# Optimization experiments

Hardware: AMD Instinct MI355X
Metric: run time of the kernel (lower is better)

Reference implementation:

```python
import jax, jax.numpy as jnp
import numpy as np

B, M, F_IN = 512, 256, 128
HID = 128          # g_feature_out_n entries
N_GL = 4           # number of GraphMatLayers
INT_D = 128
FINAL_D = 1024
OUT_DIM = 1
N_RB = 3           # ResNet block_sizes=[3]
SCALE = 0.02


def setup_inputs() -> dict:
    key = jax.random.key(0)
    ks = jax.random.split(key, 20)
    d = {}
    d['G'] = jax.random.normal(ks[0], (B, 1, M, M), dtype=jnp.float32)
    d['x_G'] = jax.random.normal(ks[1], (B, M, F_IN), dtype=jnp.float32)
    # GraphMatLayer linear weights (torch nn.Linear: [out, in]), all 128->128
    d['gml_W'] = jax.random.normal(ks[2], (N_GL, HID, F_IN), dtype=jnp.float32) * SCALE
    d['gml_b'] = jax.random.normal(ks[3], (N_GL, HID), dtype=jnp.float32) * SCALE
    d['lin0_W'] = jax.random.normal(ks[4], (INT_D, HID), dtype=jnp.float32) * SCALE
    d['lin0_b'] = jax.random.normal(ks[5], (INT_D,), dtype=jnp.float32) * SCALE
    d['rin_W'] = jax.random.normal(ks[6], (INT_D, INT_D), dtype=jnp.float32) * SCALE
    d['rin_b'] = jax.random.normal(ks[7], (INT_D,), dtype=jnp.float32) * SCALE
    d['rb1_W'] = jax.random.normal(ks[8], (N_RB, INT_D, INT_D), dtype=jnp.float32) * SCALE
    d['rb1_b'] = jax.random.normal(ks[9], (N_RB, INT_D), dtype=jnp.float32) * SCALE
    d['rb2_W'] = jax.random.normal(ks[10], (N_RB, INT_D, INT_D), dtype=jnp.float32) * SCALE
    d['rout_W'] = jax.random.normal(ks[11], (INT_D, INT_D), dtype=jnp.float32) * SCALE
    d['rout_b'] = jax.random.normal(ks[12], (INT_D,), dtype=jnp.float32) * SCALE
    d['f1_W'] = jax.random.normal(ks[13], (FINAL_D, INT_D), dtype=jnp.float32) * SCALE
    d['f1_b'] = jax.random.normal(ks[14], (FINAL_D,), dtype=jnp.float32) * SCALE
    d['f2_W'] = jax.random.normal(ks[15], (OUT_DIM, FINAL_D), dtype=jnp.float32) * SCALE
    d['f2_b'] = jax.random.normal(ks[16], (OUT_DIM,), dtype=jnp.float32) * SCALE
    return d


def reference(G, x_G, gml_W, gml_b, lin0_W, lin0_b, rin_W, rin_b,
              rb1_W, rb1_b, rb2_W, rout_W, rout_b, f1_W, f1_b, f2_W, f2_b):
    # GS=1: G[:, 0] is the per-graph adjacency [B, M, M].
    # Note: with GS=1 the torch code's resnet shape check never matches
    # (extra singleton dims accumulate), so there are NO residuals in gml.
    G0 = G[:, 0]
    x = x_G  # [B, M, C]
    for l in range(gml_W.shape[0]):  # static small loop over layers
        y = x @ gml_W[l].T + gml_b[l]             # linear projection [B,M,P]
        x = jax.nn.relu(jnp.einsum('bmn,bnp->bmp', G0, y))
    h = x.reshape(-1, x.shape[-1])                # [B*M, HID]
    h = h @ lin0_W.T + lin0_b                     # Linear(D, INT_D)
    h = h @ rin_W.T + rin_b                       # ResNet.linear_in
    for i in range(rb1_W.shape[0]):               # 3 residual blocks
        h = h + jax.nn.relu(h @ rb1_W[i].T + rb1_b[i]) @ rb2_W[i].T
    h = h @ rout_W.T + rout_b                     # ResNet.linear_out
    h = jax.nn.relu(h @ f1_W.T + f1_b)            # Linear(INT_D, FINAL_D) + ReLU
    out = h @ f2_W.T + f2_b                       # Linear(FINAL_D, OUT_DIM)
    return out.reshape(G.shape[0], G.shape[2], -1)  # [B, M, OUT_DIM]
```

## Files before the change

kernel.cpp:

```cpp
#include <hip/hip_runtime.h>


typedef __attribute__((ext_vector_type(8))) __bf16 bf16x8;
typedef __attribute__((ext_vector_type(4))) float f32x4;
typedef __attribute__((ext_vector_type(4))) unsigned short us4;
typedef __attribute__((ext_vector_type(8))) unsigned short us8;

#define MFMA16(a, b, c) __builtin_amdgcn_mfma_f32_16x16x32_bf16((a), (b), (c), 0, 0, 0)

__device__ __forceinline__ unsigned short f2bf(float f) {
  unsigned u = __float_as_uint(f);
  return (unsigned short)((u + 0x7fffu + ((u >> 16) & 1u)) >> 16);
}
__device__ __forceinline__ float bf2f(unsigned short s) {
  return __uint_as_float(((unsigned)s) << 16);
}
__device__ __forceinline__ bf16x8 asb(us8 u) { return __builtin_bit_cast(bf16x8, u); }

__device__ __forceinline__ us8 cvt8(f32x4 a, f32x4 c) {
  us8 r;
  r[0] = f2bf(a[0]); r[1] = f2bf(a[1]); r[2] = f2bf(a[2]); r[3] = f2bf(a[3]);
  r[4] = f2bf(c[0]); r[5] = f2bf(c[1]); r[6] = f2bf(c[2]); r[7] = f2bf(c[3]);
  return r;
}

__device__ __forceinline__ bf16x8 lds_frag(const unsigned short* p) {
  return asb(*reinterpret_cast<const us8*>(p));
}

struct WReg { f32x4 a[4]; f32x4 b[4]; };

__device__ __forceinline__ void stage_load(WReg& w, const float* __restrict__ src, int tid) {
#pragma unroll
  for (int it = 0; it < 4; ++it) {
    int o = tid + it * 512;
    int p = o >> 4;
    int f = (o & 15) << 3;
    const float* s = src + p * 128 + f;
    w.a[it] = *reinterpret_cast<const f32x4*>(s);
    w.b[it] = *reinterpret_cast<const f32x4*>(s + 4);
  }
}

__device__ __forceinline__ void stage_store(const WReg& w, unsigned short* dst, int tid) {
#pragma unroll
  for (int it = 0; it < 4; ++it) {
    int o = tid + it * 512;
    int p = o >> 4;
    int f = (o & 15) << 3;
    *reinterpret_cast<us8*>(&dst[p * 128 + (f ^ ((p & 7) << 3))]) = cvt8(w.a[it], w.b[it]);
  }
}

__global__ __launch_bounds__(512, 2)
void fused_model(const float* __restrict__ G, const float* __restrict__ xG,
                 const float* __restrict__ gmlW, const float* __restrict__ gmlb,
                 const float* __restrict__ lin0W, const float* __restrict__ lin0b,
                 const float* __restrict__ rinW, const float* __restrict__ rinb,
                 const float* __restrict__ rb1W, const float* __restrict__ rb1b,
                 const float* __restrict__ rb2W,
                 const float* __restrict__ routW, const float* __restrict__ routb,
                 const float* __restrict__ f1W, const float* __restrict__ f1b,
                 const float* __restrict__ f2W, const float* __restrict__ f2b,
                 float* __restrict__ out)
{
  __shared__ __align__(16) unsigned short bufA[256 * 128];
  __shared__ __align__(16) unsigned short bufB[256 * 128];
  __shared__ __align__(16) unsigned short wls[128 * 128];

  const int tid = (int)threadIdx.x;
  const int b = (int)blockIdx.x;
  const int wv = tid >> 6;
  const int lane = tid & 63;
  const int lr = lane & 15;
  const int lg = lane >> 4;

  const f32x4 zero4 = {0.f, 0.f, 0.f, 0.f};
  WReg wreg;

  {
    const float* xb = xG + (size_t)b * (256 * 128);
#pragma unroll
    for (int it = 0; it < 8; ++it) {
      int o = tid + it * 512;
      int n = o >> 4;
      int f = (o & 15) << 3;
      const float* s = xb + n * 128 + f;
      f32x4 x0 = *reinterpret_cast<const f32x4*>(s);
      f32x4 x1 = *reinterpret_cast<const f32x4*>(s + 4);
      *reinterpret_cast<us8*>(&bufA[n * 128 + (f ^ ((n & 7) << 3))]) = cvt8(x0, x1);
    }
  }
  stage_load(wreg, gmlW, tid);
  stage_store(wreg, wls, tid);

  const float* Gb = G + (size_t)b * (256 * 256);
  bf16x8 bg[2][8];
#pragma unroll
  for (int mt = 0; mt < 2; ++mt) {
    int m = wv * 32 + mt * 16 + lr;
    const float* grow = Gb + (size_t)m * 256;
#pragma unroll
    for (int ks = 0; ks < 8; ++ks) {
      const float* s = grow + ks * 32 + lg * 8;
      f32x4 x0 = *reinterpret_cast<const f32x4*>(s);
      f32x4 x1 = *reinterpret_cast<const f32x4*>(s + 4);
      bg[mt][ks] = asb(cvt8(x0, x1));
    }
  }
  __syncthreads();

#pragma unroll 1
  for (int l = 0; l < 4; ++l) {
    {
      bf16x8 a[2][4];
#pragma unroll
      for (int nt = 0; nt < 2; ++nt) {
        int n = wv * 32 + nt * 16 + lr;
#pragma unroll
        for (int k = 0; k < 4; ++k)
          a[nt][k] = lds_frag(&bufA[n * 128 + ((k * 32 + lg * 8) ^ ((n & 7) << 3))]);
      }
      const float* bias = gmlb + l * 128;
#pragma unroll
      for (int ptg = 0; ptg < 8; ptg += 4) {
        f32x4 acc[4][2];
#pragma unroll
        for (int j = 0; j < 4; ++j) { acc[j][0] = zero4; acc[j][1] = zero4; }
#pragma unroll
        for (int k = 0; k < 4; ++k) {
#pragma unroll
          for (int j = 0; j < 4; ++j) {
            int p = (ptg + j) * 16 + lr;
            bf16x8 bw = lds_frag(&wls[p * 128 + ((k * 32 + lg * 8) ^ ((p & 7) << 3))]);
            acc[j][0] = MFMA16(a[0][k], bw, acc[j][0]);
            acc[j][1] = MFMA16(a[1][k], bw, acc[j][1]);
          }
        }
#pragma unroll
        for (int j = 0; j < 4; ++j) {
          int p = (ptg + j) * 16 + lr;
          float bv = bias[p];
#pragma unroll
          for (int nt = 0; nt < 2; ++nt) {
            int nb = wv * 32 + nt * 16 + lg * 4;
            us4 pk;
#pragma unroll
            for (int r = 0; r < 4; ++r) pk[r] = f2bf(acc[j][nt][r] + bv);
            *reinterpret_cast<us4*>(&bufB[p * 256 + (nb ^ ((p & 7) << 3))]) = pk;
          }
        }
      }
    }
    __syncthreads();

    stage_load(wreg, (l < 3) ? (gmlW + (l + 1) * 16384) : lin0W, tid);

    {
#pragma unroll
      for (int ptg = 0; ptg < 8; ptg += 2) {
        bf16x8 ya[2][8];
#pragma unroll
        for (int j = 0; j < 2; ++j) {
          int p = (ptg + j) * 16 + lr;
#pragma unroll
          for (int ks = 0; ks < 8; ++ks)
            ya[j][ks] = lds_frag(&bufB[p * 256 + ((ks * 32 + lg * 8) ^ ((p & 7) << 3))]);
        }
        f32x4 acc[2][2];
        acc[0][0] = zero4; acc[0][1] = zero4; acc[1][0] = zero4; acc[1][1] = zero4;
#pragma unroll
        for (int ks = 0; ks < 8; ++ks) {
#pragma unroll
          for (int j = 0; j < 2; ++j) {
            acc[j][0] = MFMA16(ya[j][ks], bg[0][ks], acc[j][0]);
            acc[j][1] = MFMA16(ya[j][ks], bg[1][ks], acc[j][1]);
          }
        }
#pragma unroll
        for (int j = 0; j < 2; ++j) {
#pragma unroll
          for (int mt = 0; mt < 2; ++mt) {
            int m = wv * 32 + mt * 16 + lr;
            int pb = (ptg + j) * 16 + lg * 4;
            us4 pk;
#pragma unroll
            for (int r = 0; r < 4; ++r) {
              float v = acc[j][mt][r];
              v = v > 0.f ? v : 0.f;
              pk[r] = f2bf(v);
            }
            *reinterpret_cast<us4*>(&bufA[m * 128 + (pb ^ ((m & 7) << 3))]) = pk;
          }
        }
      }
    }
    stage_store(wreg, wls, tid);
    __syncthreads();
  }

  stage_load(wreg, rinW, tid);
#pragma unroll 1
  for (int op = 0; op < 9; ++op) {
    const float* bp;
    const float* wn;
    bool rl = false, rs = false;
    switch (op) {
      case 0: bp = lin0b;      wn = rb1W;          break;
      case 1: bp = rinb;       wn = rb2W;          break;
      case 2: bp = rb1b;       wn = rb1W + 16384;  rl = true; break;
      case 3: bp = nullptr;    wn = rb2W + 16384;  rs = true; break;
      case 4: bp = rb1b + 128; wn = rb1W + 32768;  rl = true; break;
      case 5: bp = nullptr;    wn = rb2W + 32768;  rs = true; break;
      case 6: bp = rb1b + 256; wn = routW;         rl = true; break;
      case 7: bp = nullptr;    wn = f1W;           rs = true; break;
      default: bp = routb;     wn = nullptr;       break;
    }
    const unsigned short* s = (op & 1) ? bufB : bufA;
    unsigned short* d = (op & 1) ? bufA : bufB;

    bf16x8 hb[2][4];
#pragma unroll
    for (int nt = 0; nt < 2; ++nt) {
      int n = wv * 32 + nt * 16 + lr;
#pragma unroll
      for (int k = 0; k < 4; ++k)
        hb[nt][k] = lds_frag(&s[n * 128 + ((k * 32 + lg * 8) ^ ((n & 7) << 3))]);
    }
#pragma unroll
    for (int ptg = 0; ptg < 8; ptg += 4) {
      f32x4 acc[4][2];
#pragma unroll
      for (int j = 0; j < 4; ++j) { acc[j][0] = zero4; acc[j][1] = zero4; }
#pragma unroll
      for (int k = 0; k < 4; ++k) {
#pragma unroll
        for (int j = 0; j < 4; ++j) {
          int p = (ptg + j) * 16 + lr;
          bf16x8 aw = lds_frag(&wls[p * 128 + ((k * 32 + lg * 8) ^ ((p & 7) << 3))]);
          acc[j][0] = MFMA16(aw, hb[0][k], acc[j][0]);
          acc[j][1] = MFMA16(aw, hb[1][k], acc[j][1]);
        }
      }
#pragma unroll
      for (int j = 0; j < 4; ++j) {
        int p0 = (ptg + j) * 16 + lg * 4;
        f32x4 bv = bp ? *reinterpret_cast<const f32x4*>(&bp[p0]) : zero4;
#pragma unroll
        for (int nt = 0; nt < 2; ++nt) {
          int n = wv * 32 + nt * 16 + lr;
          int idx = n * 128 + (p0 ^ ((n & 7) << 3));
          us4 pk;
          if (rs) {
            us4 old = *reinterpret_cast<const us4*>(&d[idx]);
#pragma unroll
            for (int r = 0; r < 4; ++r) pk[r] = f2bf(acc[j][nt][r] + bf2f(old[r]));
          } else if (rl) {
#pragma unroll
            for (int r = 0; r < 4; ++r) {
              float v = acc[j][nt][r] + bv[r];
              pk[r] = f2bf(v > 0.f ? v : 0.f);
            }
          } else {
#pragma unroll
            for (int r = 0; r < 4; ++r) pk[r] = f2bf(acc[j][nt][r] + bv[r]);
          }
          *reinterpret_cast<us4*>(&d[idx]) = pk;
        }
      }
    }
    __syncthreads();
    stage_store(wreg, wls, tid);
    __syncthreads();
    if (op < 8) stage_load(wreg, wn, tid);
  }

  {
    bf16x8 a[2][4];
#pragma unroll
    for (int nt = 0; nt < 2; ++nt) {
      int n = wv * 32 + nt * 16 + lr;
#pragma unroll
      for (int k = 0; k < 4; ++k)
        a[nt][k] = lds_frag(&bufB[n * 128 + ((k * 32 + lg * 8) ^ ((n & 7) << 3))]);
    }
    float oacc[2][4];
#pragma unroll
    for (int nt = 0; nt < 2; ++nt)
#pragma unroll
      for (int r = 0; r < 4; ++r) oacc[nt][r] = 0.f;

    stage_load(wreg, f1W + 16384, tid);

#pragma unroll 1
    for (int c = 0; c < 8; ++c) {
      const unsigned short* wc = (c & 1) ? bufA : wls;
      unsigned short* wother = (c & 1) ? wls : bufA;
      if (c < 7) stage_store(wreg, wother, tid);
#pragma unroll
      for (int ptg = 0; ptg < 8; ptg += 2) {
        f32x4 acc[2][2];
        acc[0][0] = zero4; acc[0][1] = zero4; acc[1][0] = zero4; acc[1][1] = zero4;
#pragma unroll
        for (int k = 0; k < 4; ++k) {
#pragma unroll
          for (int j = 0; j < 2; ++j) {
            int p = (ptg + j) * 16 + lr;
            bf16x8 bw = lds_frag(&wc[p * 128 + ((k * 32 + lg * 8) ^ ((p & 7) << 3))]);
            acc[j][0] = MFMA16(a[0][k], bw, acc[j][0]);
            acc[j][1] = MFMA16(a[1][k], bw, acc[j][1]);
          }
        }
#pragma unroll
        for (int j = 0; j < 2; ++j) {
          int kg = c * 128 + (ptg + j) * 16 + lr;
          float b1 = f1b[kg];
          float w2 = f2W[kg];
#pragma unroll
          for (int nt = 0; nt < 2; ++nt) {
#pragma unroll
            for (int r = 0; r < 4; ++r) {
              float v = acc[j][nt][r] + b1;
              v = v > 0.f ? v : 0.f;
              oacc[nt][r] += v * w2;
            }
          }
        }
      }
      __syncthreads();
      if (c < 6) stage_load(wreg, f1W + (c + 2) * 16384, tid);
    }

#pragma unroll
    for (int msk = 1; msk < 16; msk <<= 1) {
#pragma unroll
      for (int nt = 0; nt < 2; ++nt)
#pragma unroll
        for (int r = 0; r < 4; ++r)
          oacc[nt][r] += __shfl_xor(oacc[nt][r], msk, 64);
    }
    if (lr == 0) {
      float fb = f2b[0];
#pragma unroll
      for (int nt = 0; nt < 2; ++nt)
#pragma unroll
        for (int r = 0; r < 4; ++r)
          out[b * 256 + wv * 32 + nt * 16 + lg * 4 + r] = oacc[nt][r] + fb;
    }
  }
}

extern "C" void kernel_launch(void* const* d_in, const int* in_sizes, int n_in,
                              void* d_out, int out_size, void* d_ws, size_t ws_size,
                              hipStream_t stream) {
  (void)in_sizes; (void)n_in; (void)d_ws; (void)ws_size; (void)out_size;
  fused_model<<<512, 512, 0, stream>>>(
      (const float*)d_in[0],  (const float*)d_in[1],
      (const float*)d_in[2],  (const float*)d_in[3],
      (const float*)d_in[4],  (const float*)d_in[5],
      (const float*)d_in[6],  (const float*)d_in[7],
      (const float*)d_in[8],  (const float*)d_in[9],
      (const float*)d_in[10],
      (const float*)d_in[11], (const float*)d_in[12],
      (const float*)d_in[13], (const float*)d_in[14],
      (const float*)d_in[15], (const float*)d_in[16],
      (float*)d_out);
}
```

Baseline: 426.3 us.

## Double block to 1024 threads, splitting output columns across wave pairs

Grows the workgroup from 8 to 16 waves. Each pair of waves shares a 32-row slab, and each wave of the pair computes half of the output-feature tiles in every GEMM stage. Per-wave work and register footprint shrink, so more waves are available to hide MFMA and LDS latency. The final per-row reduction now sums two wave partials through LDS, which adds an extra barrier. The bf16 conversion also switches to the compiler's native __bf16 cast, and launch bounds now request 4 waves per SIMD, which caps registers per thread.

```diff
diff --git a/kernel.cpp b/kernel.cpp
--- a/kernel.cpp
+++ b/kernel.cpp
@@ -9,8 +9,7 @@
 #define MFMA16(a, b, c) __builtin_amdgcn_mfma_f32_16x16x32_bf16((a), (b), (c), 0, 0, 0)
 
 __device__ __forceinline__ unsigned short f2bf(float f) {
-  unsigned u = __float_as_uint(f);
-  return (unsigned short)((u + 0x7fffu + ((u >> 16) & 1u)) >> 16);
+  return __builtin_bit_cast(unsigned short, static_cast<__bf16>(f));
 }
 __device__ __forceinline__ float bf2f(unsigned short s) {
   return __uint_as_float(((unsigned)s) << 16);
@@ -28,12 +27,12 @@
   return asb(*reinterpret_cast<const us8*>(p));
 }
 
-struct WReg { f32x4 a[4]; f32x4 b[4]; };
+struct WReg { f32x4 a[2]; f32x4 b[2]; };
 
 __device__ __forceinline__ void stage_load(WReg& w, const float* __restrict__ src, int tid) {
 #pragma unroll
-  for (int it = 0; it < 4; ++it) {
-    int o = tid + it * 512;
+  for (int it = 0; it < 2; ++it) {
+    int o = tid + it * 1024;
     int p = o >> 4;
     int f = (o & 15) << 3;
     const float* s = src + p * 128 + f;
@@ -44,15 +43,15 @@
 
 __device__ __forceinline__ void stage_store(const WReg& w, unsigned short* dst, int tid) {
 #pragma unroll
-  for (int it = 0; it < 4; ++it) {
-    int o = tid + it * 512;
+  for (int it = 0; it < 2; ++it) {
+    int o = tid + it * 1024;
     int p = o >> 4;
     int f = (o & 15) << 3;
     *reinterpret_cast<us8*>(&dst[p * 128 + (f ^ ((p & 7) << 3))]) = cvt8(w.a[it], w.b[it]);
   }
 }
 
-__global__ __launch_bounds__(512, 2)
+__global__ __launch_bounds__(1024, 4)
 void fused_model(const float* __restrict__ G, const float* __restrict__ xG,
                  const float* __restrict__ gmlW, const float* __restrict__ gmlb,
                  const float* __restrict__ lin0W, const float* __restrict__ lin0b,
@@ -71,6 +70,8 @@
   const int tid = (int)threadIdx.x;
   const int b = (int)blockIdx.x;
   const int wv = tid >> 6;
+  const int wr = wv >> 1;
+  const int wp = wv & 1;
   const int lane = tid & 63;
   const int lr = lane & 15;
   const int lg = lane >> 4;
@@ -81,8 +82,8 @@
   {
     const float* xb = xG + (size_t)b * (256 * 128);
 #pragma unroll
-    for (int it = 0; it < 8; ++it) {
-      int o = tid + it * 512;
+    for (int it = 0; it < 4; ++it) {
+      int o = tid + it * 1024;
       int n = o >> 4;
       int f = (o & 15) << 3;
       const float* s = xb + n * 128 + f;
@@ -98,7 +99,7 @@
   bf16x8 bg[2][8];
 #pragma unroll
   for (int mt = 0; mt < 2; ++mt) {
-    int m = wv * 32 + mt * 16 + lr;
+    int m = wr * 32 + mt * 16 + lr;
     const float* grow = Gb + (size_t)m * 256;
 #pragma unroll
     for (int ks = 0; ks < 8; ++ks) {
@@ -116,73 +117,70 @@
       bf16x8 a[2][4];
 #pragma unroll
       for (int nt = 0; nt < 2; ++nt) {
-        int n = wv * 32 + nt * 16 + lr;
+        int n = wr * 32 + nt * 16 + lr;
 #pragma unroll
         for (int k = 0; k < 4; ++k)
           a[nt][k] = lds_frag(&bufA[n * 128 + ((k * 32 + lg * 8) ^ ((n & 7) << 3))]);
       }
       const float* bias = gmlb + l * 128;
 #pragma unroll
-      for (int ptg = 0; ptg < 8; ptg += 4) {
-        f32x4 acc[4][2];
-#pragma unroll
-        for (int j = 0; j < 4; ++j) { acc[j][0] = zero4; acc[j][1] = zero4; }
-#pragma unroll
-        for (int k = 0; k < 4; ++k) {
-#pragma unroll
-          for (int j = 0; j < 4; ++j) {
-            int p = (ptg + j) * 16 + lr;
-            bf16x8 bw = lds_frag(&wls[p * 128 + ((k * 32 + lg * 8) ^ ((p & 7) << 3))]);
-            acc[j][0] = MFMA16(a[0][k], bw, acc[j][0]);
-            acc[j][1] = MFMA16(a[1][k], bw, acc[j][1]);
-          }
-        }
-#pragma unroll
-        for (int j = 0; j < 4; ++j) {
-          int p = (ptg + j) * 16 + lr;
-          float bv = bias[p];
-#pragma unroll
-          for (int nt = 0; nt < 2; ++nt) {
-            int nb = wv * 32 + nt * 16 + lg * 4;
-            us4 pk;
-#pragma unroll
-            for (int r = 0; r < 4; ++r) pk[r] = f2bf(acc[j][nt][r] + bv);
-            *reinterpret_cast<us4*>(&bufB[p * 256 + (nb ^ ((p & 7) << 3))]) = pk;
-          }
-        }
-      }
-    }
-    __syncthreads();
-
-    stage_load(wreg, (l < 3) ? (gmlW + (l + 1) * 16384) : lin0W, tid);
-
-    {
-#pragma unroll
-      for (int ptg = 0; ptg < 8; ptg += 2) {
-        bf16x8 ya[2][8];
-#pragma unroll
-        for (int j = 0; j < 2; ++j) {
-          int p = (ptg + j) * 16 + lr;
-#pragma unroll
-          for (int ks = 0; ks < 8; ++ks)
-            ya[j][ks] = lds_frag(&bufB[p * 256 + ((ks * 32 + lg * 8) ^ ((p & 7) << 3))]);
-        }
+      for (int jg = 0; jg < 4; jg += 2) {
         f32x4 acc[2][2];
         acc[0][0] = zero4; acc[0][1] = zero4; acc[1][0] = zero4; acc[1][1] = zero4;
 #pragma unroll
+        for (int k = 0; k < 4; ++k) {
+#pragma unroll
+          for (int jj = 0; jj < 2; ++jj) {
+            int p = (wp * 4 + jg + jj) * 16 + lr;
+            bf16x8 bw = lds_frag(&wls[p * 128 + ((k * 32 + lg * 8) ^ ((p & 7) << 3))]);
+            acc[jj][0] = MFMA16(a[0][k], bw, acc[jj][0]);
+            acc[jj][1] = MFMA16(a[1][k], bw, acc[jj][1]);
+          }
+        }
+#pragma unroll
+        for (int jj = 0; jj < 2; ++jj) {
+          int p = (wp * 4 + jg + jj) * 16 + lr;
+          float bv = bias[p];
+#pragma unroll
+          for (int nt = 0; nt < 2; ++nt) {
+            int nb = wr * 32 + nt * 16 + lg * 4;
+            us4 pk;
+#pragma unroll
+            for (int r = 0; r < 4; ++r) pk[r] = f2bf(acc[jj][nt][r] + bv);
+            *reinterpret_cast<us4*>(&bufB[p * 256 + (nb ^ ((p & 7) << 3))]) = pk;
+          }
+        }
+      }
+    }
+    __syncthreads();
+
+    stage_load(wreg, (l < 3) ? (gmlW + (l + 1) * 16384) : lin0W, tid);
+
+    {
+#pragma unroll
+      for (int jj = 0; jj < 2; ++jj) {
+        f32x4 acc[2][2];
+        acc[0][0] = zero4; acc[0][1] = zero4; acc[1][0] = zero4; acc[1][1] = zero4;
+#pragma unroll
         for (int ks = 0; ks < 8; ++ks) {
+          bf16x8 ya[2];
 #pragma unroll
           for (int j = 0; j < 2; ++j) {
-            acc[j][0] = MFMA16(ya[j][ks], bg[0][ks], acc[j][0]);
-            acc[j][1] = MFMA16(ya[j][ks], bg[1][ks], acc[j][1]);
+            int p = (wp * 4 + jj * 2 + j) * 16 + lr;
+            ya[j] = lds_frag(&bufB[p * 256 + ((ks * 32 + lg * 8) ^ ((p & 7) << 3))]);
+          }
+#pragma unroll
+          for (int j = 0; j < 2; ++j) {
+            acc[j][0] = MFMA16(ya[j], bg[0][ks], acc[j][0]);
+            acc[j][1] = MFMA16(ya[j], bg[1][ks], acc[j][1]);
           }
         }
 #pragma unroll
         for (int j = 0; j < 2; ++j) {
 #pragma unroll
           for (int mt = 0; mt < 2; ++mt) {
-            int m = wv * 32 + mt * 16 + lr;
-            int pb = (ptg + j) * 16 + lg * 4;
+            int m = wr * 32 + mt * 16 + lr;
+            int pb = (wp * 4 + jj * 2 + j) * 16 + lg * 4;
             us4 pk;
 #pragma unroll
             for (int r = 0; r < 4; ++r) {
@@ -222,51 +220,48 @@
     bf16x8 hb[2][4];
 #pragma unroll
     for (int nt = 0; nt < 2; ++nt) {
-      int n = wv * 32 + nt * 16 + lr;
+      int n = wr * 32 + nt * 16 + lr;
 #pragma unroll
       for (int k = 0; k < 4; ++k)
         hb[nt][k] = lds_frag(&s[n * 128 + ((k * 32 + lg * 8) ^ ((n & 7) << 3))]);
     }
-#pragma unroll
-    for (int ptg = 0; ptg < 8; ptg += 4) {
-      f32x4 acc[4][2];
-#pragma unroll
-      for (int j = 0; j < 4; ++j) { acc[j][0] = zero4; acc[j][1] = zero4; }
-#pragma unroll
-      for (int k = 0; k < 4; ++k) {
-#pragma unroll
-        for (int j = 0; j < 4; ++j) {
-          int p = (ptg + j) * 16 + lr;
-          bf16x8 aw = lds_frag(&wls[p * 128 + ((k * 32 + lg * 8) ^ ((p & 7) << 3))]);
-          acc[j][0] = MFMA16(aw, hb[0][k], acc[j][0]);
-          acc[j][1] = MFMA16(aw, hb[1][k], acc[j][1]);
-        }
-      }
+    f32x4 acc[4][2];
+#pragma unroll
+    for (int j = 0; j < 4; ++j) { acc[j][0] = zero4; acc[j][1] = zero4; }
+#pragma unroll
+    for (int k = 0; k < 4; ++k) {
 #pragma unroll
       for (int j = 0; j < 4; ++j) {
-        int p0 = (ptg + j) * 16 + lg * 4;
-        f32x4 bv = bp ? *reinterpret_cast<const f32x4*>(&bp[p0]) : zero4;
-#pragma unroll
-        for (int nt = 0; nt < 2; ++nt) {
-          int n = wv * 32 + nt * 16 + lr;
-          int idx = n * 128 + (p0 ^ ((n & 7) << 3));
-          us4 pk;
-          if (rs) {
-            us4 old = *reinterpret_cast<const us4*>(&d[idx]);
-#pragma unroll
-            for (int r = 0; r < 4; ++r) pk[r] = f2bf(acc[j][nt][r] + bf2f(old[r]));
-          } else if (rl) {
-#pragma unroll
-            for (int r = 0; r < 4; ++r) {
-              float v = acc[j][nt][r] + bv[r];
-              pk[r] = f2bf(v > 0.f ? v : 0.f);
-            }
-          } else {
-#pragma unroll
-            for (int r = 0; r < 4; ++r) pk[r] = f2bf(acc[j][nt][r] + bv[r]);
-          }
-          *reinterpret_cast<us4*>(&d[idx]) = pk;
-        }
+        int p = (wp * 4 + j) * 16 + lr;
+        bf16x8 aw = lds_frag(&wls[p * 128 + ((k * 32 + lg * 8) ^ ((p & 7) << 3))]);
+        acc[j][0] = MFMA16(aw, hb[0][k], acc[j][0]);
+        acc[j][1] = MFMA16(aw, hb[1][k], acc[j][1]);
+      }
+    }
+#pragma unroll
+    for (int j = 0; j < 4; ++j) {
+      int p0 = (wp * 4 + j) * 16 + lg * 4;
+      f32x4 bv = bp ? *reinterpret_cast<const f32x4*>(&bp[p0]) : zero4;
+#pragma unroll
+      for (int nt = 0; nt < 2; ++nt) {
+        int n = wr * 32 + nt * 16 + lr;
+        int idx = n * 128 + (p0 ^ ((n & 7) << 3));
+        us4 pk;
+        if (rs) {
+          us4 old = *reinterpret_cast<const us4*>(&d[idx]);
+#pragma unroll
+          for (int r = 0; r < 4; ++r) pk[r] = f2bf(acc[j][nt][r] + bf2f(old[r]));
+        } else if (rl) {
+#pragma unroll
+          for (int r = 0; r < 4; ++r) {
+            float v = acc[j][nt][r] + bv[r];
+            pk[r] = f2bf(v > 0.f ? v : 0.f);
+          }
+        } else {
+#pragma unroll
+          for (int r = 0; r < 4; ++r) pk[r] = f2bf(acc[j][nt][r] + bv[r]);
+        }
+        *reinterpret_cast<us4*>(&d[idx]) = pk;
       }
     }
     __syncthreads();
@@ -279,7 +274,7 @@
     bf16x8 a[2][4];
 #pragma unroll
     for (int nt = 0; nt < 2; ++nt) {
-      int n = wv * 32 + nt * 16 + lr;
+      int n = wr * 32 + nt * 16 + lr;
 #pragma unroll
       for (int k = 0; k < 4; ++k)
         a[nt][k] = lds_frag(&bufB[n * 128 + ((k * 32 + lg * 8) ^ ((n & 7) << 3))]);
@@ -297,33 +292,31 @@
       const unsigned short* wc = (c & 1) ? bufA : wls;
       unsigned short* wother = (c & 1) ? wls : bufA;
       if (c < 7) stage_store(wreg, wother, tid);
-#pragma unroll
-      for (int ptg = 0; ptg < 8; ptg += 2) {
-        f32x4 acc[2][2];
-        acc[0][0] = zero4; acc[0][1] = zero4; acc[1][0] = zero4; acc[1][1] = zero4;
-#pragma unroll
-        for (int k = 0; k < 4; ++k) {
-#pragma unroll
-          for (int j = 0; j < 2; ++j) {
-            int p = (ptg + j) * 16 + lr;
-            bf16x8 bw = lds_frag(&wc[p * 128 + ((k * 32 + lg * 8) ^ ((p & 7) << 3))]);
-            acc[j][0] = MFMA16(a[0][k], bw, acc[j][0]);
-            acc[j][1] = MFMA16(a[1][k], bw, acc[j][1]);
-          }
-        }
-#pragma unroll
-        for (int j = 0; j < 2; ++j) {
-          int kg = c * 128 + (ptg + j) * 16 + lr;
-          float b1 = f1b[kg];
-          float w2 = f2W[kg];
-#pragma unroll
-          for (int nt = 0; nt < 2; ++nt) {
-#pragma unroll
-            for (int r = 0; r < 4; ++r) {
-              float v = acc[j][nt][r] + b1;
-              v = v > 0.f ? v : 0.f;
-              oacc[nt][r] += v * w2;
-            }
+      f32x4 acc[4][2];
+#pragma unroll
+      for (int j = 0; j < 4; ++j) { acc[j][0] = zero4; acc[j][1] = zero4; }
+#pragma unroll
+      for (int k = 0; k < 4; ++k) {
+#pragma unroll
+        for (int j = 0; j < 4; ++j) {
+          int p = (wp * 4 + j) * 16 + lr;
+          bf16x8 bw = lds_frag(&wc[p * 128 + ((k * 32 + lg * 8) ^ ((p & 7) << 3))]);
+          acc[j][0] = MFMA16(a[0][k], bw, acc[j][0]);
+          acc[j][1] = MFMA16(a[1][k], bw, acc[j][1]);
+        }
+      }
+#pragma unroll
+      for (int j = 0; j < 4; ++j) {
+        int kg = c * 128 + (wp * 4 + j) * 16 + lr;
+        float b1 = f1b[kg];
+        float w2 = f2W[kg];
+#pragma unroll
+        for (int nt = 0; nt < 2; ++nt) {
+#pragma unroll
+          for (int r = 0; r < 4; ++r) {
+            float v = acc[j][nt][r] + b1;
+            v = v > 0.f ? v : 0.f;
+            oacc[nt][r] += v * w2;
           }
         }
       }
@@ -339,13 +332,24 @@
         for (int r = 0; r < 4; ++r)
           oacc[nt][r] += __shfl_xor(oacc[nt][r], msk, 64);
     }
+    float* pf = reinterpret_cast<float*>(wls);
     if (lr == 0) {
+#pragma unroll
+      for (int nt = 0; nt < 2; ++nt)
+#pragma unroll
+        for (int r = 0; r < 4; ++r)
+          pf[wp * 256 + wr * 32 + nt * 16 + lg * 4 + r] = oacc[nt][r];
+    }
+    __syncthreads();
+    if (lr == 0 && wp == 0) {
       float fb = f2b[0];
 #pragma unroll
       for (int nt = 0; nt < 2; ++nt)
 #pragma unroll
-        for (int r = 0; r < 4; ++r)
-          out[b * 256 + wv * 32 + nt * 16 + lg * 4 + r] = oacc[nt][r] + fb;
+        for (int r = 0; r < 4; ++r) {
+          int row = wr * 32 + nt * 16 + lg * 4 + r;
+          out[b * 256 + row] = pf[row] + pf[256 + row] + fb;
+        }
     }
   }
 }
@@ -354,7 +358,7 @@
                               void* d_out, int out_size, void* d_ws, size_t ws_size,
                               hipStream_t stream) {
   (void)in_sizes; (void)n_in; (void)d_ws; (void)ws_size; (void)out_size;
-  fused_model<<<512, 512, 0, stream>>>(
+  fused_model<<<512, 1024, 0, stream>>>(
       (const float*)d_in[0],  (const float*)d_in[1],
       (const float*)d_in[2],  (const float*)d_in[3],
       (const float*)d_in[4],  (const float*)d_in[5],
```

After: 444.7 us. 1.04x slower.
